# Optimization experiments

Hardware: AMD Instinct MI355X
Metric: run time of the kernel (lower is better)

Reference implementation:

```python
import jax, jax.numpy as jnp
import numpy as np

B, T, C, H = 2, 2048, 2048, 16
HD = C // H  # head_dim = 128


def setup_inputs() -> dict:
    key = jax.random.key(0)
    k1, k2, k3 = jax.random.split(key, 3)
    x = jax.random.normal(k1, (B, T, C), dtype=jnp.float32)
    # causal mask: positions with mask==0 are blocked (masked_fill(mask==0, -inf))
    mask = jnp.tril(jnp.ones((T, T), dtype=bool))[None, None]  # [1,1,T,T]
    W_qkv = jax.random.normal(k2, (C, 3 * C), dtype=jnp.float32) * (C ** -0.5)
    W_proj = jax.random.normal(k3, (C, C), dtype=jnp.float32) * (C ** -0.5)
    b_proj = jnp.zeros((C,), dtype=jnp.float32)
    return {"x": x, "mask": mask, "W_qkv": W_qkv, "W_proj": W_proj, "b_proj": b_proj}


def reference(x, mask, W_qkv, W_proj, b_proj):
    # QKV projection (Linear, bias=False)
    qkv = jnp.einsum('btc,cd->btd', x, W_qkv)            # [B,T,3C]
    qkv = qkv.reshape(B, T, 3, H, HD)
    q = qkv[:, :, 0].transpose(0, 2, 1, 3)               # [B,H,T,HD]
    k = qkv[:, :, 1].transpose(0, 2, 1, 3)
    v = qkv[:, :, 2].transpose(0, 2, 1, 3)
    # scaled dot-product attention (dropout is identity in eval)
    att = jnp.einsum('bhqd,bhkd->bhqk', q, k) / jnp.sqrt(jnp.float32(HD))
    att = jnp.where(mask, att, -jnp.inf)
    att = jax.nn.softmax(att, axis=-1)
    y = jnp.einsum('bhqk,bhkd->bhqd', att, v)            # [B,H,T,HD]
    y = y.transpose(0, 2, 1, 3).reshape(B, T, C)
    return jnp.einsum('btc,cd->btd', y, W_proj) + b_proj
```

## Files before the change

### kernel.cpp

```cpp
#include <hip/hip_runtime.h>
#include <hip/hip_bf16.h>

#define B_  2
#define T_  2048
#define C_  2048
#define H_  16
#define HD_ 128

using bf16x8 = __attribute__((ext_vector_type(8))) __bf16;
using f32x4  = __attribute__((ext_vector_type(4))) float;

__device__ __forceinline__ unsigned short f2bs(float f) {
    __hip_bfloat16 h = __float2bfloat16(f);
    return __builtin_bit_cast(unsigned short, h);
}

__device__ __forceinline__ void gload_lds16(const unsigned short* g, unsigned short* l) {
    __builtin_amdgcn_global_load_lds(
        (const __attribute__((address_space(1))) unsigned int*)g,
        (__attribute__((address_space(3))) unsigned int*)l, 16, 0, 0);
}

__global__ __launch_bounds__(256) void k_prep(const float* __restrict__ x,
                                              unsigned short* __restrict__ XB,
                                              const float* __restrict__ Wqkv,
                                              unsigned short* __restrict__ WQKVT,
                                              const float* __restrict__ Wproj,
                                              unsigned short* __restrict__ WPROJT) {
    __shared__ unsigned short t[64][65];
    int blk = blockIdx.x;
    int tid = threadIdx.x;
    if (blk < 8192) {
        int i = blk * 256 + tid;
        float4 v = reinterpret_cast<const float4*>(x)[i];
        ushort4 o;
        o.x = f2bs(v.x); o.y = f2bs(v.y); o.z = f2bs(v.z); o.w = f2bs(v.w);
        reinterpret_cast<ushort4*>(XB)[i] = o;
        return;
    }
    const float* in;
    unsigned short* out;
    int K = 2048, N, bx, by;
    if (blk < 11264) {
        in = Wqkv; out = WQKVT; N = 6144;
        bx = (blk - 8192) % 96; by = (blk - 8192) / 96;
    } else {
        in = Wproj; out = WPROJT; N = 2048;
        bx = (blk - 11264) % 32; by = (blk - 11264) / 32;
    }
    int k0 = by * 64, n0 = bx * 64;
#pragma unroll
    for (int p = 0; p < 4; ++p) {
        int idx = p * 256 + tid;
        int r = idx >> 4, c = (idx & 15) << 2;
        float4 v = *reinterpret_cast<const float4*>(in + (long)(k0 + r) * N + n0 + c);
        t[r][c] = f2bs(v.x); t[r][c + 1] = f2bs(v.y);
        t[r][c + 2] = f2bs(v.z); t[r][c + 3] = f2bs(v.w);
    }
    __syncthreads();
#pragma unroll
    for (int p = 0; p < 4; ++p) {
        int idx = p * 256 + tid;
        int r = idx >> 4, c = (idx & 15) << 2;
        ushort4 o;
        o.x = t[c][r]; o.y = t[c + 1][r]; o.z = t[c + 2][r]; o.w = t[c + 3][r];
        *reinterpret_cast<ushort4*>(out + (long)(n0 + r) * K + k0 + c) = o;
    }
}

template <int MODE>
__global__ __launch_bounds__(256, 2) void k_gemm(const unsigned short* __restrict__ A,
                                                 const unsigned short* __restrict__ Bt,
                                                 int M, int N, int K,
                                                 unsigned short* __restrict__ qkv,
                                                 float* __restrict__ out,
                                                 const float* __restrict__ bias) {
    __shared__ __align__(16) unsigned short lA[2][128 * 32];
    __shared__ __align__(16) unsigned short lB[2][128 * 32];

    int tid = threadIdx.x;
    int wave = tid >> 6, lane = tid & 63;
    int quad = lane >> 4, l16 = lane & 15;
    int wr = (wave >> 1) * 64, wc = (wave & 1) * 64;
    int m0 = blockIdx.y * 128, n0 = blockIdx.x * 128;

    int lrow = lane >> 2;
    int lcol = (lane & 3) << 3;
    const unsigned short* gA0 = A + (long)(m0 + wave * 32 + lrow) * K + lcol;
    const unsigned short* gA1 = A + (long)(m0 + wave * 32 + 16 + lrow) * K + lcol;
    const unsigned short* gB0 = Bt + (long)(n0 + wave * 32 + lrow) * K + lcol;
    const unsigned short* gB1 = Bt + (long)(n0 + wave * 32 + 16 + lrow) * K + lcol;
    int lofs0 = wave * 1024, lofs1 = wave * 1024 + 512;

    f32x4 zero = {0.f, 0.f, 0.f, 0.f};
    f32x4 acc[4][4];
#pragma unroll
    for (int i = 0; i < 4; ++i)
#pragma unroll
        for (int j = 0; j < 4; ++j) acc[i][j] = zero;

    for (int k0 = 0; k0 < K; k0 += 64) {
        __syncthreads();
#pragma unroll
        for (int h = 0; h < 2; ++h) {
            int kk = k0 + h * 32;
            gload_lds16(gA0 + kk, &lA[h][lofs0]);
            gload_lds16(gA1 + kk, &lA[h][lofs1]);
            gload_lds16(gB0 + kk, &lB[h][lofs0]);
            gload_lds16(gB1 + kk, &lB[h][lofs1]);
        }
        __syncthreads();
#pragma unroll
        for (int h = 0; h < 2; ++h) {
            bf16x8 af[4], bfr[4];
#pragma unroll
            for (int i = 0; i < 4; ++i)
                af[i] = *reinterpret_cast<const bf16x8*>(&lA[h][(wr + i * 16 + l16) * 32 + quad * 8]);
#pragma unroll
            for (int j = 0; j < 4; ++j)
                bfr[j] = *reinterpret_cast<const bf16x8*>(&lB[h][(wc + j * 16 + l16) * 32 + quad * 8]);
#pragma unroll
            for (int i = 0; i < 4; ++i)
#pragma unroll
                for (int j = 0; j < 4; ++j)
                    acc[i][j] = __builtin_amdgcn_mfma_f32_16x16x32_bf16(af[i], bfr[j], acc[i][j], 0, 0, 0);
        }
    }

#pragma unroll
    for (int i = 0; i < 4; ++i) {
#pragma unroll
        for (int j = 0; j < 4; ++j) {
#pragma unroll
            for (int r = 0; r < 4; ++r) {
                int m = m0 + wr + i * 16 + quad * 4 + r;
                int n = n0 + wc + j * 16 + l16;
                float v = acc[i][j][r];
                if (MODE == 0) {
                    int s = n >> 11, col = n & 2047;
                    int h = col >> 7, hd = col & 127;
                    int b = m >> 11, t = m & 2047;
                    long base = (long)s * (B_ * H_ * T_ * HD_);
                    if (s == 2)
                        qkv[base + ((long)(b * H_ + h) * HD_ + hd) * T_ + t] = f2bs(v);
                    else
                        qkv[base + ((long)(b * H_ + h) * T_ + t) * HD_ + hd] = f2bs(v);
                } else {
                    out[(long)m * N + n] = v + bias[n];
                }
            }
        }
    }
}

__global__ __launch_bounds__(256, 3) void k_attn(const unsigned short* __restrict__ qkv,
                                                 unsigned short* __restrict__ y) {
    __shared__ __align__(16) unsigned short lK[64 * 136];
    __shared__ __align__(16) unsigned short lVt[128 * 72];
    __shared__ __align__(16) unsigned short lP[4][16 * 72];

    int tid = threadIdx.x;
    int wave = tid >> 6, lane = tid & 63;
    int quad = lane >> 4, l16 = lane & 15;
    int bh = blockIdx.x;
    int qb = ((int)gridDim.y - 1 - (int)blockIdx.y) * 64;

    const unsigned short* Qh = qkv + (long)bh * (T_ * HD_);
    const unsigned short* Kh = qkv + (long)(B_ * H_) * T_ * HD_ + (long)bh * (T_ * HD_);
    const unsigned short* Vt = qkv + 2L * (B_ * H_) * T_ * HD_ + (long)bh * (HD_ * T_);

    bf16x8 aQ[4];
    int qrow = qb + wave * 16 + l16;
#pragma unroll
    for (int kk = 0; kk < 4; ++kk)
        aQ[kk] = *reinterpret_cast<const bf16x8*>(Qh + (long)qrow * HD_ + kk * 32 + quad * 8);

    float m_s[4], l_s[4];
    f32x4 O[8];
    f32x4 zero = {0.f, 0.f, 0.f, 0.f};
#pragma unroll
    for (int r = 0; r < 4; ++r) { m_s[r] = -1e30f; l_s[r] = 0.f; }
#pragma unroll
    for (int h = 0; h < 8; ++h) O[h] = zero;

    int qmax = qb + wave * 16 + 15;
    const float scl = 0.08838834764831845f;

    for (int kb = 0; kb < qb + 64; kb += 64) {
        __syncthreads();
#pragma unroll
        for (int p = 0; p < 4; ++p) {
            int id = p * 256 + tid;
            int r = id >> 4, cc = (id & 15) << 3;
            *reinterpret_cast<int4*>(&lK[r * 136 + cc]) =
                *reinterpret_cast<const int4*>(Kh + (long)(kb + r) * HD_ + cc);
        }
#pragma unroll
        for (int p = 0; p < 4; ++p) {
            int id = p * 256 + tid;
            int r = id >> 3, cc = (id & 7) << 3;
            *reinterpret_cast<int4*>(&lVt[r * 72 + cc]) =
                *reinterpret_cast<const int4*>(Vt + (long)r * T_ + kb + cc);
        }
        __syncthreads();
        if (kb > qmax) continue;

        f32x4 s[4];
#pragma unroll
        for (int st = 0; st < 4; ++st) s[st] = zero;
#pragma unroll
        for (int kk = 0; kk < 4; ++kk) {
#pragma unroll
            for (int st = 0; st < 4; ++st) {
                bf16x8 b = *reinterpret_cast<const bf16x8*>(
                    &lK[(st * 16 + l16) * 136 + kk * 32 + quad * 8]);
                s[st] = __builtin_amdgcn_mfma_f32_16x16x32_bf16(aQ[kk], b, s[st], 0, 0, 0);
            }
        }

        int qg = qb + wave * 16 + quad * 4;
#pragma unroll
        for (int r = 0; r < 4; ++r) {
            int q = qg + r;
            float x[4];
#pragma unroll
            for (int st = 0; st < 4; ++st)
                x[st] = (kb + st * 16 + l16 <= q) ? s[st][r] * scl : -1e30f;
            float mx = fmaxf(fmaxf(x[0], x[1]), fmaxf(x[2], x[3]));
#pragma unroll
            for (int off = 1; off < 16; off <<= 1) mx = fmaxf(mx, __shfl_xor(mx, off));
            float mn = fmaxf(m_s[r], mx);
            float al = __expf(m_s[r] - mn);
            float p[4], rs = 0.f;
#pragma unroll
            for (int st = 0; st < 4; ++st) { p[st] = __expf(x[st] - mn); rs += p[st]; }
#pragma unroll
            for (int off = 1; off < 16; off <<= 1) rs += __shfl_xor(rs, off);
            m_s[r] = mn;
            l_s[r] = l_s[r] * al + rs;
            int row = quad * 4 + r;
#pragma unroll
            for (int st = 0; st < 4; ++st)
                lP[wave][row * 72 + st * 16 + l16] = f2bs(p[st]);
#pragma unroll
            for (int h = 0; h < 8; ++h) O[h][r] *= al;
        }

#pragma unroll
        for (int kc = 0; kc < 2; ++kc) {
            bf16x8 pf = *reinterpret_cast<const bf16x8*>(
                &lP[wave][l16 * 72 + kc * 32 + quad * 8]);
#pragma unroll
            for (int h = 0; h < 8; ++h) {
                bf16x8 vf = *reinterpret_cast<const bf16x8*>(
                    &lVt[(h * 16 + l16) * 72 + kc * 32 + quad * 8]);
                O[h] = __builtin_amdgcn_mfma_f32_16x16x32_bf16(pf, vf, O[h], 0, 0, 0);
            }
        }
    }

    int b = bh >> 4, hh = bh & 15;
#pragma unroll
    for (int r = 0; r < 4; ++r) {
        int t = qb + wave * 16 + quad * 4 + r;
        float inv = 1.f / l_s[r];
#pragma unroll
        for (int h = 0; h < 8; ++h)
            y[(long)(b * T_ + t) * C_ + hh * HD_ + h * 16 + l16] = f2bs(O[h][r] * inv);
    }
}

extern "C" void kernel_launch(void* const* d_in, const int* in_sizes, int n_in,
                              void* d_out, int out_size, void* d_ws, size_t ws_size,
                              hipStream_t stream) {
    const float* x     = (const float*)d_in[0];
    const float* Wqkv  = (const float*)d_in[2];
    const float* Wproj = (const float*)d_in[3];
    const float* bproj = (const float*)d_in[4];
    float* out = (float*)d_out;

    unsigned short* XB     = (unsigned short*)d_ws;
    unsigned short* WQKVT  = XB + 8388608;
    unsigned short* WPROJT = WQKVT + 12582912;
    unsigned short* QKV    = WPROJT + 4194304;
    if (ws_size < 100663296) return;

    k_prep<<<12288, 256, 0, stream>>>(x, XB, Wqkv, WQKVT, Wproj, WPROJT);
    k_gemm<0><<<dim3(6144 / 128, 4096 / 128), 256, 0, stream>>>(XB, WQKVT, 4096, 6144, 2048,
                                                                QKV, nullptr, nullptr);
    k_attn<<<dim3(32, 32), 256, 0, stream>>>(QKV, XB);
    k_gemm<1><<<dim3(2048 / 128, 4096 / 128), 256, 0, stream>>>(XB, WPROJT, 4096, 2048, 2048,
                                                                nullptr, out, bproj);
}
```

Measured before the change: 404.2 us.

## Use 256x256-tile 8-wave GEMM with 4-stage LDS pipeline for QKV projection

Adds a new QKV GEMM kernel that uses 256x256 output tiles with 512 threads, a 4-deep LDS ring buffer fed by direct global-to-LDS loads, XOR-swizzled LDS addressing, and split MFMA phases separated by barriers with raised wave priority. It replaces the 128x128 tile kernel for the QKV projection, aiming for more operand reuse per LDS load and better overlap of memory loads with matrix math. The grid shrinks to 384 blocks, which may leave CUs unevenly loaded, and the larger tile raises register and LDS pressure.

```diff
diff --git a/kernel.cpp b/kernel.cpp
--- a/kernel.cpp
+++ b/kernel.cpp
@@ -153,6 +153,117 @@
     }
 }
 
+__global__ __launch_bounds__(512, 2) void k_gemm256(const unsigned short* __restrict__ A,
+                                                    const unsigned short* __restrict__ Bt,
+                                                    int M, int N, int K,
+                                                    unsigned short* __restrict__ qkv) {
+    __shared__ __align__(16) unsigned short lA[4][256 * 32];
+    __shared__ __align__(16) unsigned short lB[4][256 * 32];
+
+    const int tid = threadIdx.x;
+    const int wave = tid >> 6, lane = tid & 63;
+    const int quad = lane >> 4, l16 = lane & 15;
+    const int wm = wave >> 2, wn = wave & 3;
+    const int m0 = blockIdx.y * 256, n0 = blockIdx.x * 256;
+
+    const int srow  = lane >> 2;
+    const int scole = ((((lane & 3) << 4) ^ (((lane >> 3) & 3) << 4)) >> 1);
+    const unsigned short* gA0 = A + (long)(m0 + wave * 32 + srow) * K + scole;
+    const unsigned short* gA1 = gA0 + 16L * K;
+    const unsigned short* gB0 = Bt + (long)(n0 + wave * 32 + srow) * K + scole;
+    const unsigned short* gB1 = gB0 + 16L * K;
+    const int ld0 = wave * 1024, ld1 = wave * 1024 + 512;
+
+    const int kofs = ((quad ^ ((l16 >> 1) & 3)) << 3);
+    const int arow = wm * 128 + l16;
+    const int brow = wn * 64 + l16;
+
+    f32x4 zero = {0.f, 0.f, 0.f, 0.f};
+    f32x4 acc[8][4];
+#pragma unroll
+    for (int i = 0; i < 8; ++i)
+#pragma unroll
+        for (int j = 0; j < 4; ++j) acc[i][j] = zero;
+
+    const int NT = K >> 5;
+
+    gload_lds16(gA0, &lA[0][ld0]); gload_lds16(gB0, &lB[0][ld0]);
+    gload_lds16(gA1, &lA[0][ld1]); gload_lds16(gB1, &lB[0][ld1]);
+    gload_lds16(gA0 + 32, &lA[1][ld0]); gload_lds16(gB0 + 32, &lB[1][ld0]);
+    gload_lds16(gA1 + 32, &lA[1][ld1]); gload_lds16(gB1 + 32, &lB[1][ld1]);
+    asm volatile("s_waitcnt vmcnt(4)" ::: "memory");
+    asm volatile("s_barrier" ::: "memory");
+
+#pragma unroll 4
+    for (int t = 0; t < NT; ++t) {
+        const int buf = t & 3, pb = (t + 2) & 3;
+        const bool pf = (t + 2) < NT;
+        const long ko = (long)(t + 2) << 5;
+
+        bf16x8 af[4], bfr[4];
+#pragma unroll
+        for (int i = 0; i < 4; ++i)
+            af[i] = *reinterpret_cast<const bf16x8*>(&lA[buf][(arow + i * 16) * 32 + kofs]);
+#pragma unroll
+        for (int j = 0; j < 4; ++j)
+            bfr[j] = *reinterpret_cast<const bf16x8*>(&lB[buf][(brow + j * 16) * 32 + kofs]);
+        if (pf) {
+            gload_lds16(gA0 + ko, &lA[pb][ld0]);
+            gload_lds16(gB0 + ko, &lB[pb][ld0]);
+        }
+        asm volatile("s_barrier" ::: "memory");
+        __builtin_amdgcn_s_setprio(1);
+#pragma unroll
+        for (int i = 0; i < 4; ++i)
+#pragma unroll
+            for (int j = 0; j < 4; ++j)
+                acc[i][j] = __builtin_amdgcn_mfma_f32_16x16x32_bf16(af[i], bfr[j], acc[i][j], 0, 0, 0);
+        __builtin_amdgcn_s_setprio(0);
+        asm volatile("s_barrier" ::: "memory");
+
+#pragma unroll
+        for (int i = 0; i < 4; ++i)
+            af[i] = *reinterpret_cast<const bf16x8*>(&lA[buf][(arow + (4 + i) * 16) * 32 + kofs]);
+        if (pf) {
+            gload_lds16(gA1 + ko, &lA[pb][ld1]);
+            gload_lds16(gB1 + ko, &lB[pb][ld1]);
+            asm volatile("s_waitcnt vmcnt(4)" ::: "memory");
+        } else {
+            asm volatile("s_waitcnt vmcnt(0)" ::: "memory");
+        }
+        asm volatile("s_barrier" ::: "memory");
+        __builtin_amdgcn_s_setprio(1);
+#pragma unroll
+        for (int i = 0; i < 4; ++i)
+#pragma unroll
+            for (int j = 0; j < 4; ++j)
+                acc[4 + i][j] = __builtin_amdgcn_mfma_f32_16x16x32_bf16(af[i], bfr[j], acc[4 + i][j], 0, 0, 0);
+        __builtin_amdgcn_s_setprio(0);
+        asm volatile("s_barrier" ::: "memory");
+    }
+
+#pragma unroll
+    for (int i = 0; i < 8; ++i) {
+#pragma unroll
+        for (int j = 0; j < 4; ++j) {
+#pragma unroll
+            for (int r = 0; r < 4; ++r) {
+                int m = m0 + wm * 128 + i * 16 + quad * 4 + r;
+                int n = n0 + wn * 64 + j * 16 + l16;
+                float v = acc[i][j][r];
+                int s = n >> 11, col = n & 2047;
+                int h = col >> 7, hd = col & 127;
+                int b = m >> 11, tt = m & 2047;
+                long base = (long)s * (B_ * H_ * T_ * HD_);
+                if (s == 2)
+                    qkv[base + ((long)(b * H_ + h) * HD_ + hd) * T_ + tt] = f2bs(v);
+                else
+                    qkv[base + ((long)(b * H_ + h) * T_ + tt) * HD_ + hd] = f2bs(v);
+            }
+        }
+    }
+}
+
 __global__ __launch_bounds__(256, 3) void k_attn(const unsigned short* __restrict__ qkv,
                                                  unsigned short* __restrict__ y) {
     __shared__ __align__(16) unsigned short lK[64 * 136];
@@ -286,8 +397,7 @@
     if (ws_size < 100663296) return;
 
     k_prep<<<12288, 256, 0, stream>>>(x, XB, Wqkv, WQKVT, Wproj, WPROJT);
-    k_gemm<0><<<dim3(6144 / 128, 4096 / 128), 256, 0, stream>>>(XB, WQKVT, 4096, 6144, 2048,
-                                                                QKV, nullptr, nullptr);
+    k_gemm256<<<dim3(6144 / 256, 4096 / 256), 512, 0, stream>>>(XB, WQKVT, 4096, 6144, 2048, QKV);
     k_attn<<<dim3(32, 32), 256, 0, stream>>>(QKV, XB);
     k_gemm<1><<<dim3(2048 / 128, 4096 / 128), 256, 0, stream>>>(XB, WPROJT, 4096, 2048, 2048,
                                                                 nullptr, out, bproj);
```

New measurement: 421.1 us. 4.2% more time.

## Register-prefetch next K/V tile and transpose S MFMA for lane-local softmax

Applied to the files above, without the earlier changes.

The attention kernel now loads the next K and V tile into registers while the current tile is computed, then writes the registers to LDS at the top of the next iteration. This hides global-load latency behind compute. The QK^T MFMA operands are swapped so each lane holds one query's scores, which cuts the 16-lane shuffle reductions to two shuffles and lets P be written to LDS as packed 4-wide stores. The costs are more registers, raw s_barrier/waitcnt asm in place of __syncthreads, and removal of the early-skip branch for fully masked tiles.

```diff
diff --git a/kernel.cpp b/kernel.cpp
--- a/kernel.cpp
+++ b/kernel.cpp
@@ -19,6 +19,10 @@
     __builtin_amdgcn_global_load_lds(
         (const __attribute__((address_space(1))) unsigned int*)g,
         (__attribute__((address_space(3))) unsigned int*)l, 16, 0, 0);
+}
+
+__device__ __forceinline__ void barrier_fenced() {
+    asm volatile("s_barrier" ::: "memory");
 }
 
 __global__ __launch_bounds__(256) void k_prep(const float* __restrict__ x,
@@ -175,35 +179,57 @@
     for (int kk = 0; kk < 4; ++kk)
         aQ[kk] = *reinterpret_cast<const bf16x8*>(Qh + (long)qrow * HD_ + kk * 32 + quad * 8);
 
-    float m_s[4], l_s[4];
+    int4 kreg[4], vreg[4];
+#pragma unroll
+    for (int p = 0; p < 4; ++p) {
+        int id = p * 256 + tid;
+        int kr = id >> 4, kc = (id & 15) << 3;
+        kreg[p] = *reinterpret_cast<const int4*>(Kh + (long)kr * HD_ + kc);
+        int vr = id >> 3, vc = (id & 7) << 3;
+        vreg[p] = *reinterpret_cast<const int4*>(Vt + (long)vr * T_ + vc);
+    }
+
+    float m_l = -1e30f, l_l = 0.f;
     f32x4 O[8];
     f32x4 zero = {0.f, 0.f, 0.f, 0.f};
 #pragma unroll
-    for (int r = 0; r < 4; ++r) { m_s[r] = -1e30f; l_s[r] = 0.f; }
-#pragma unroll
     for (int h = 0; h < 8; ++h) O[h] = zero;
 
-    int qmax = qb + wave * 16 + 15;
+    const int q_abs = qb + wave * 16 + l16;
     const float scl = 0.08838834764831845f;
-
-    for (int kb = 0; kb < qb + 64; kb += 64) {
-        __syncthreads();
+    const int kbend = qb + 64;
+
+    for (int kb = 0; kb < kbend; kb += 64) {
+        barrier_fenced();
+
 #pragma unroll
         for (int p = 0; p < 4; ++p) {
             int id = p * 256 + tid;
-            int r = id >> 4, cc = (id & 15) << 3;
-            *reinterpret_cast<int4*>(&lK[r * 136 + cc]) =
-                *reinterpret_cast<const int4*>(Kh + (long)(kb + r) * HD_ + cc);
+            int kr = id >> 4, kc = (id & 15) << 3;
+            *reinterpret_cast<int4*>(&lK[kr * 136 + kc]) = kreg[p];
         }
 #pragma unroll
         for (int p = 0; p < 4; ++p) {
             int id = p * 256 + tid;
-            int r = id >> 3, cc = (id & 7) << 3;
-            *reinterpret_cast<int4*>(&lVt[r * 72 + cc]) =
-                *reinterpret_cast<const int4*>(Vt + (long)r * T_ + kb + cc);
-        }
-        __syncthreads();
-        if (kb > qmax) continue;
+            int vr = id >> 3, vc = (id & 7) << 3;
+            *reinterpret_cast<int4*>(&lVt[vr * 72 + vc]) = vreg[p];
+        }
+
+        {
+            int nkb = kb + 64;
+            long ko = (nkb < kbend) ? nkb : 0;
+#pragma unroll
+            for (int p = 0; p < 4; ++p) {
+                int id = p * 256 + tid;
+                int kr = id >> 4, kc = (id & 15) << 3;
+                kreg[p] = *reinterpret_cast<const int4*>(Kh + (ko + kr) * HD_ + kc);
+                int vr = id >> 3, vc = (id & 7) << 3;
+                vreg[p] = *reinterpret_cast<const int4*>(Vt + (long)vr * T_ + ko + vc);
+            }
+        }
+
+        asm volatile("s_waitcnt lgkmcnt(0)" ::: "memory");
+        barrier_fenced();
 
         f32x4 s[4];
 #pragma unroll
@@ -212,39 +238,56 @@
         for (int kk = 0; kk < 4; ++kk) {
 #pragma unroll
             for (int st = 0; st < 4; ++st) {
-                bf16x8 b = *reinterpret_cast<const bf16x8*>(
+                bf16x8 kf = *reinterpret_cast<const bf16x8*>(
                     &lK[(st * 16 + l16) * 136 + kk * 32 + quad * 8]);
-                s[st] = __builtin_amdgcn_mfma_f32_16x16x32_bf16(aQ[kk], b, s[st], 0, 0, 0);
-            }
-        }
-
-        int qg = qb + wave * 16 + quad * 4;
-#pragma unroll
-        for (int r = 0; r < 4; ++r) {
-            int q = qg + r;
-            float x[4];
-#pragma unroll
-            for (int st = 0; st < 4; ++st)
-                x[st] = (kb + st * 16 + l16 <= q) ? s[st][r] * scl : -1e30f;
-            float mx = fmaxf(fmaxf(x[0], x[1]), fmaxf(x[2], x[3]));
-#pragma unroll
-            for (int off = 1; off < 16; off <<= 1) mx = fmaxf(mx, __shfl_xor(mx, off));
-            float mn = fmaxf(m_s[r], mx);
-            float al = __expf(m_s[r] - mn);
-            float p[4], rs = 0.f;
-#pragma unroll
-            for (int st = 0; st < 4; ++st) { p[st] = __expf(x[st] - mn); rs += p[st]; }
-#pragma unroll
-            for (int off = 1; off < 16; off <<= 1) rs += __shfl_xor(rs, off);
-            m_s[r] = mn;
-            l_s[r] = l_s[r] * al + rs;
-            int row = quad * 4 + r;
-#pragma unroll
-            for (int st = 0; st < 4; ++st)
-                lP[wave][row * 72 + st * 16 + l16] = f2bs(p[st]);
-#pragma unroll
-            for (int h = 0; h < 8; ++h) O[h][r] *= al;
-        }
+                s[st] = __builtin_amdgcn_mfma_f32_16x16x32_bf16(kf, aQ[kk], s[st], 0, 0, 0);
+            }
+        }
+
+        float xv[4][4];
+        float mx = -1e30f;
+#pragma unroll
+        for (int st = 0; st < 4; ++st)
+#pragma unroll
+            for (int r = 0; r < 4; ++r) {
+                int key = kb + st * 16 + quad * 4 + r;
+                float v = (key <= q_abs) ? s[st][r] * scl : -1e30f;
+                xv[st][r] = v;
+                mx = fmaxf(mx, v);
+            }
+        mx = fmaxf(mx, __shfl_xor(mx, 16));
+        mx = fmaxf(mx, __shfl_xor(mx, 32));
+        float mn = fmaxf(m_l, mx);
+        float al = __expf(m_l - mn);
+        float rs = 0.f;
+#pragma unroll
+        for (int st = 0; st < 4; ++st)
+#pragma unroll
+            for (int r = 0; r < 4; ++r) {
+                float e = __expf(xv[st][r] - mn);
+                xv[st][r] = e;
+                rs += e;
+            }
+        rs += __shfl_xor(rs, 16);
+        rs += __shfl_xor(rs, 32);
+        m_l = mn;
+        l_l = l_l * al + rs;
+
+#pragma unroll
+        for (int st = 0; st < 4; ++st) {
+            ushort4 pk;
+            pk.x = f2bs(xv[st][0]); pk.y = f2bs(xv[st][1]);
+            pk.z = f2bs(xv[st][2]); pk.w = f2bs(xv[st][3]);
+            *reinterpret_cast<ushort4*>(&lP[wave][l16 * 72 + st * 16 + quad * 4]) = pk;
+        }
+
+        float alr[4];
+#pragma unroll
+        for (int r = 0; r < 4; ++r) alr[r] = __shfl(al, quad * 4 + r);
+#pragma unroll
+        for (int h = 0; h < 8; ++h)
+#pragma unroll
+            for (int r = 0; r < 4; ++r) O[h][r] *= alr[r];
 
 #pragma unroll
         for (int kc = 0; kc < 2; ++kc) {
@@ -263,7 +306,7 @@
 #pragma unroll
     for (int r = 0; r < 4; ++r) {
         int t = qb + wave * 16 + quad * 4 + r;
-        float inv = 1.f / l_s[r];
+        float inv = 1.f / __shfl(l_l, quad * 4 + r);
 #pragma unroll
         for (int h = 0; h < 8; ++h)
             y[(long)(b * T_ + t) * C_ + hh * HD_ + h * 16 + l16] = f2bs(O[h][r] * inv);
```

After: 481.3 us. 19.1% more time.
